# Kernel tuning notes

Hardware: AMD Instinct MI355X
Metric: run time of the kernel (lower is better)

Reference implementation:

```python
import jax, jax.numpy as jnp
import numpy as np

NUM_HEADS = 16
HEAD_DIM = 64
D_DEC = 1024
D_ENC = 1024
R = 256  # kv_lora_rank
LN_EPS = 1e-5


def setup_inputs() -> dict:
    key = jax.random.key(0)
    ks = jax.random.split(key, 8)
    B, SQ, SK = 4, 2048, 4096
    query = jax.random.normal(ks[0], (B, SQ, D_DEC), dtype=jnp.float32)
    encoder_output = jax.random.normal(ks[1], (B, SK, D_ENC), dtype=jnp.float32)
    s = 0.02
    Wq = jax.random.normal(ks[2], (NUM_HEADS * HEAD_DIM, D_DEC), dtype=jnp.float32) * s
    Wkva = jax.random.normal(ks[3], (R, D_ENC), dtype=jnp.float32) * s
    ln_g = jnp.ones((R,), dtype=jnp.float32)
    ln_b = jnp.zeros((R,), dtype=jnp.float32)
    Wkvb = jax.random.normal(ks[4], (NUM_HEADS * 2 * HEAD_DIM, R), dtype=jnp.float32) * s
    Wout = jax.random.normal(ks[5], (D_DEC, NUM_HEADS * HEAD_DIM), dtype=jnp.float32) * s
    return {"query": query, "encoder_output": encoder_output, "Wq": Wq,
            "Wkva": Wkva, "ln_g": ln_g, "ln_b": ln_b, "Wkvb": Wkvb, "Wout": Wout}


def reference(query, encoder_output, Wq, Wkva, ln_g, ln_b, Wkvb, Wout):
    B, SQ, _ = query.shape
    SK = encoder_output.shape[1]
    H, Dh = NUM_HEADS, HEAD_DIM

    # q projection -> [B, H, SQ, Dh]
    q = jnp.einsum('bsd,ed->bse', query, Wq).reshape(B, SQ, H, Dh).transpose(0, 2, 1, 3)

    # low-rank KV compression + layernorm
    c = jnp.einsum('bsd,rd->bsr', encoder_output, Wkva)  # [B, SK, R]
    mu = jnp.mean(c, axis=-1, keepdims=True)
    var = jnp.mean(jnp.square(c - mu), axis=-1, keepdims=True)
    c = (c - mu) * jax.lax.rsqrt(var + LN_EPS) * ln_g + ln_b

    # decompress to K,V: [B, SK, H, 2*Dh] -> split
    kv = jnp.einsum('bsr,er->bse', c, Wkvb).reshape(B, SK, H, 2 * Dh).transpose(0, 2, 1, 3)
    k, v = kv[..., :Dh], kv[..., Dh:]

    scale = 1.0 / np.sqrt(Dh).astype(np.float32)
    scores = jnp.einsum('bhqd,bhkd->bhqk', q, k) * scale
    attn = jax.nn.softmax(scores, axis=-1)  # dropout is identity in eval / p=0
    o = jnp.einsum('bhqk,bhkd->bhqd', attn, v)
    o = o.transpose(0, 2, 1, 3).reshape(B, SQ, H * Dh)
    return jnp.einsum('bse,de->bsd', o, Wout)
```

## Files before the change

### kernel.cpp

```cpp
#include <hip/hip_runtime.h>

#define LOG2E 1.4426950408889634f

typedef __attribute__((ext_vector_type(8))) short short8;
typedef __attribute__((ext_vector_type(4))) float f32x4;

__device__ inline unsigned short f2bf(float f) {
  unsigned u = __float_as_uint(f);
  u += 0x7fffu + ((u >> 16) & 1u);
  return (unsigned short)(u >> 16);
}

#define MFMA16(a, b, c) __builtin_amdgcn_mfma_f32_16x16x32_bf16((a), (b), (c), 0, 0, 0)

#define GLDS16(gp, lp)                                                              \
  __builtin_amdgcn_global_load_lds((const __attribute__((address_space(1))) void*)(gp), \
                                   (__attribute__((address_space(3))) void*)(lp), 16, 0, 0)

__device__ inline f32x4 zero4() {
  f32x4 z = {0.f, 0.f, 0.f, 0.f};
  return z;
}

__device__ inline int swz8(int row) { return (row ^ (row >> 3)) & 7; }

__global__ __launch_bounds__(256) void k_cast(const float* __restrict__ in,
                                              unsigned short* __restrict__ out, int n) {
  int i = (blockIdx.x * 256 + threadIdx.x) * 4;
  if (i >= n) return;
  float4 v = *(const float4*)(in + i);
  unsigned lo = (unsigned)f2bf(v.x) | ((unsigned)f2bf(v.y) << 16);
  unsigned hi = (unsigned)f2bf(v.z) | ((unsigned)f2bf(v.w) << 16);
  *(uint2*)(out + i) = make_uint2(lo, hi);
}

__global__ __launch_bounds__(256, 2) void k_qproj(const unsigned short* __restrict__ A,
                                                  const unsigned short* __restrict__ Bw,
                                                  unsigned short* __restrict__ Qout) {
  __shared__ __align__(16) short As[128 * 32];
  __shared__ __align__(16) short Bs[128 * 32];
  const int K = 1024;
  int tid = threadIdx.x;
  int w = tid >> 6, lane = tid & 63, quad = lane >> 4, c = lane & 15;
  int m0 = blockIdx.x * 128, n0 = blockIdx.y * 128;
  int wm = (w >> 1) * 64, wn = (w & 1) * 64;
  f32x4 acc[4][4];
#pragma unroll
  for (int i = 0; i < 4; i++)
#pragma unroll
    for (int j = 0; j < 4; j++) acc[i][j] = zero4();

  for (int k0 = 0; k0 < K; k0 += 32) {
#pragma unroll
    for (int i = 0; i < 2; i++) {
      int seg = w * 2 + i;
      int bo = seg * 1024 + lane * 16;
      int row = bo >> 6, col = (bo & 63) >> 1;
      GLDS16(A + (size_t)(m0 + row) * K + k0 + col, (char*)As + seg * 1024);
      GLDS16(Bw + (size_t)(n0 + row) * K + k0 + col, (char*)Bs + seg * 1024);
    }
    __syncthreads();
    short8 af[4], bfr[4];
#pragma unroll
    for (int i = 0; i < 4; i++) {
      af[i] = *(const short8*)&As[(wm + i * 16 + c) * 32 + quad * 8];
      bfr[i] = *(const short8*)&Bs[(wn + i * 16 + c) * 32 + quad * 8];
    }
#pragma unroll
    for (int mi = 0; mi < 4; mi++)
#pragma unroll
      for (int ni = 0; ni < 4; ni++) acc[mi][ni] = MFMA16(af[mi], bfr[ni], acc[mi][ni]);
    __syncthreads();
  }
  const float scale = 0.125f * LOG2E;
#pragma unroll
  for (int mi = 0; mi < 4; mi++) {
    int rowb = m0 + wm + mi * 16 + quad * 4;
#pragma unroll
    for (int ni = 0; ni < 4; ni++) {
      int col = n0 + wn + ni * 16 + c;
      int h = col >> 6, d = col & 63;
#pragma unroll
      for (int r = 0; r < 4; r++) {
        int row = rowb + r;
        int b = row >> 11, sq = row & 2047;
        Qout[(((size_t)(b * 16 + h)) * 2048 + sq) * 64 + d] = f2bf(acc[mi][ni][r] * scale);
      }
    }
  }
}

__global__ __launch_bounds__(256, 2) void k_cln(const unsigned short* __restrict__ E,
                                                const unsigned short* __restrict__ Wa,
                                                const float* __restrict__ g, const float* __restrict__ bb,
                                                unsigned short* __restrict__ Cout) {
  __shared__ __align__(16) short As[64 * 32];
  __shared__ __align__(16) short Bs[256 * 32];
  __shared__ float redS[4][64], redQ[4][64];
  __shared__ float gS[256], bS[256];
  const int K = 1024;
  int tid = threadIdx.x;
  int w = tid >> 6, lane = tid & 63, quad = lane >> 4, c = lane & 15;
  int m0 = blockIdx.x * 64;
  gS[tid] = g[tid];
  bS[tid] = bb[tid];
  f32x4 acc[4][4];
#pragma unroll
  for (int i = 0; i < 4; i++)
#pragma unroll
    for (int j = 0; j < 4; j++) acc[i][j] = zero4();

  for (int k0 = 0; k0 < K; k0 += 32) {
    {
      int bo = w * 1024 + lane * 16;
      int row = bo >> 6, col = (bo & 63) >> 1;
      GLDS16(E + (size_t)(m0 + row) * K + k0 + col, (char*)As + w * 1024);
    }
#pragma unroll
    for (int i = 0; i < 4; i++) {
      int seg = w * 4 + i;
      int bo = seg * 1024 + lane * 16;
      int row = bo >> 6, col = (bo & 63) >> 1;
      GLDS16(Wa + (size_t)row * K + k0 + col, (char*)Bs + seg * 1024);
    }
    __syncthreads();
    short8 af[4], bfr[4];
#pragma unroll
    for (int i = 0; i < 4; i++) {
      af[i] = *(const short8*)&As[(i * 16 + c) * 32 + quad * 8];
      bfr[i] = *(const short8*)&Bs[(w * 64 + i * 16 + c) * 32 + quad * 8];
    }
#pragma unroll
    for (int mi = 0; mi < 4; mi++)
#pragma unroll
      for (int ni = 0; ni < 4; ni++) acc[mi][ni] = MFMA16(af[mi], bfr[ni], acc[mi][ni]);
    __syncthreads();
  }
  float ps[4][4], pq[4][4];
#pragma unroll
  for (int mi = 0; mi < 4; mi++)
#pragma unroll
    for (int r = 0; r < 4; r++) {
      float s = 0.f, q = 0.f;
#pragma unroll
      for (int ni = 0; ni < 4; ni++) {
        float x = acc[mi][ni][r];
        s += x;
        q += x * x;
      }
      for (int m = 1; m < 16; m <<= 1) {
        s += __shfl_xor(s, m, 64);
        q += __shfl_xor(q, m, 64);
      }
      ps[mi][r] = s;
      pq[mi][r] = q;
    }
  if (c == 0) {
#pragma unroll
    for (int mi = 0; mi < 4; mi++)
#pragma unroll
      for (int r = 0; r < 4; r++) {
        int row = mi * 16 + quad * 4 + r;
        redS[w][row] = ps[mi][r];
        redQ[w][row] = pq[mi][r];
      }
  }
  __syncthreads();
  float muv[4][4], rsv[4][4];
#pragma unroll
  for (int mi = 0; mi < 4; mi++)
#pragma unroll
    for (int r = 0; r < 4; r++) {
      int row = mi * 16 + quad * 4 + r;
      float S = redS[0][row] + redS[1][row] + redS[2][row] + redS[3][row];
      float Q = redQ[0][row] + redQ[1][row] + redQ[2][row] + redQ[3][row];
      float mu = S * (1.f / 256.f);
      float var = Q * (1.f / 256.f) - mu * mu;
      muv[mi][r] = mu;
      rsv[mi][r] = rsqrtf(var + 1e-5f);
    }
#pragma unroll
  for (int mi = 0; mi < 4; mi++)
#pragma unroll
    for (int ni = 0; ni < 4; ni++) {
      int col = w * 64 + ni * 16 + c;
#pragma unroll
      for (int r = 0; r < 4; r++) {
        int row = m0 + mi * 16 + quad * 4 + r;
        float y = (acc[mi][ni][r] - muv[mi][r]) * rsv[mi][r] * gS[col] + bS[col];
        Cout[(size_t)row * 256 + col] = f2bf(y);
      }
    }
}

__global__ __launch_bounds__(256, 2) void k_kv(const unsigned short* __restrict__ A,
                                               const unsigned short* __restrict__ Bw,
                                               unsigned short* __restrict__ Kb,
                                               unsigned short* __restrict__ Vb) {
  __shared__ __align__(16) short As[128 * 32];
  __shared__ __align__(16) short Bs[128 * 32];
  const int K = 256;
  int tid = threadIdx.x;
  int w = tid >> 6, lane = tid & 63, quad = lane >> 4, c = lane & 15;
  int m0 = blockIdx.x * 128, n0 = blockIdx.y * 128;
  int wm = (w >> 1) * 64, wn = (w & 1) * 64;
  f32x4 acc[4][4];
#pragma unroll
  for (int i = 0; i < 4; i++)
#pragma unroll
    for (int j = 0; j < 4; j++) acc[i][j] = zero4();

  for (int k0 = 0; k0 < K; k0 += 32) {
#pragma unroll
    for (int i = 0; i < 2; i++) {
      int seg = w * 2 + i;
      int bo = seg * 1024 + lane * 16;
      int row = bo >> 6, col = (bo & 63) >> 1;
      GLDS16(A + (size_t)(m0 + row) * K + k0 + col, (char*)As + seg * 1024);
      GLDS16(Bw + (size_t)(n0 + row) * K + k0 + col, (char*)Bs + seg * 1024);
    }
    __syncthreads();
    short8 af[4], bfr[4];
#pragma unroll
    for (int i = 0; i < 4; i++) {
      af[i] = *(const short8*)&As[(wm + i * 16 + c) * 32 + quad * 8];
      bfr[i] = *(const short8*)&Bs[(wn + i * 16 + c) * 32 + quad * 8];
    }
#pragma unroll
    for (int mi = 0; mi < 4; mi++)
#pragma unroll
      for (int ni = 0; ni < 4; ni++) acc[mi][ni] = MFMA16(af[mi], bfr[ni], acc[mi][ni]);
    __syncthreads();
  }
#pragma unroll
  for (int mi = 0; mi < 4; mi++) {
    int rowb = m0 + wm + mi * 16 + quad * 4;
#pragma unroll
    for (int ni = 0; ni < 4; ni++) {
      int col = n0 + wn + ni * 16 + c;
      int h = col >> 7, rr = col & 127;
#pragma unroll
      for (int r = 0; r < 4; r++) {
        int row = rowb + r;
        int b = row >> 12, sk = row & 4095;
        float x = acc[mi][ni][r];
        if (rr < 64)
          Kb[(((size_t)(b * 16 + h)) * 4096 + sk) * 64 + rr] = f2bf(x);
        else
          Vb[(((size_t)(b * 16 + h)) * 64 + (rr - 64)) * 4096 + sk] = f2bf(x);
      }
    }
  }
}

__global__ __launch_bounds__(256, 2) void k_attn(const unsigned short* __restrict__ Qb,
                                                 const unsigned short* __restrict__ Kb,
                                                 const unsigned short* __restrict__ Vb,
                                                 unsigned short* __restrict__ Ob) {
  __shared__ __align__(16) short Qs[256 * 64];
  __shared__ __align__(16) short Ks[64 * 64];
  __shared__ __align__(16) short Vs[64 * 64];
  int tid = threadIdx.x;
  int w = tid >> 6, lane = tid & 63, quad = lane >> 4, c = lane & 15;
  int r8 = lane >> 3, pc = lane & 7;
  int bh = blockIdx.y, qt = blockIdx.x;
  const unsigned short* Qp = Qb + ((size_t)bh * 2048 + qt * 256) * 64;
  const unsigned short* Kp = Kb + (size_t)bh * 4096 * 64;
  const unsigned short* Vp = Vb + (size_t)bh * 64 * 4096;

#pragma unroll
  for (int i = 0; i < 8; i++) {
    int seg = w * 8 + i;
    int row = seg * 8 + r8;
    int lc = pc ^ swz8(row);
    GLDS16(Qp + (size_t)row * 64 + lc * 8, (char*)Qs + seg * 1024);
  }
  __syncthreads();
  short8 qf[4][2];
#pragma unroll
  for (int nt = 0; nt < 4; nt++) {
    int row = w * 64 + nt * 16 + c;
#pragma unroll
    for (int kk = 0; kk < 2; kk++)
      qf[nt][kk] = *(const short8*)((const char*)Qs + row * 128 + (((kk * 4 + quad) ^ swz8(row)) << 4));
  }
  char* PsW = (char*)Qs + w * 8192;

  f32x4 O[4][4];
  float lp[4] = {0.f, 0.f, 0.f, 0.f};
#pragma unroll
  for (int i = 0; i < 4; i++)
#pragma unroll
    for (int j = 0; j < 4; j++) O[i][j] = zero4();

  for (int kt = 0; kt < 64; kt++) {
#pragma unroll
    for (int i = 0; i < 4; i++) {
      int seg = w * 4 + i;
      if (seg < 8) {
        int row = seg * 8 + r8;
        int lc = pc ^ swz8(row);
        GLDS16(Kp + ((size_t)kt * 64 + row) * 64 + lc * 8, (char*)Ks + seg * 1024);
      } else {
        int row = (seg - 8) * 8 + r8;
        int lc = pc ^ swz8(row);
        GLDS16(Vp + (size_t)row * 4096 + kt * 64 + lc * 8, (char*)Vs + (seg - 8) * 1024);
      }
    }
    __syncthreads();

#pragma unroll
    for (int mt = 0; mt < 4; mt++) {
      int krow = mt * 16 + c;
      short8 kf0 = *(const short8*)((const char*)Ks + krow * 128 + ((quad ^ swz8(krow)) << 4));
      short8 kf1 = *(const short8*)((const char*)Ks + krow * 128 + (((4 + quad) ^ swz8(krow)) << 4));
      f32x4 s[4];
#pragma unroll
      for (int nt = 0; nt < 4; nt++) {
        s[nt] = MFMA16(kf0, qf[nt][0], zero4());
        s[nt] = MFMA16(kf1, qf[nt][1], s[nt]);
      }
#pragma unroll
      for (int nt = 0; nt < 4; nt++) {
        float p0 = __builtin_amdgcn_exp2f(s[nt][0]);
        float p1 = __builtin_amdgcn_exp2f(s[nt][1]);
        float p2 = __builtin_amdgcn_exp2f(s[nt][2]);
        float p3 = __builtin_amdgcn_exp2f(s[nt][3]);
        lp[nt] += (p0 + p1) + (p2 + p3);
        unsigned u0 = ((__float_as_uint(p0) + 0x8000u) >> 16) | ((__float_as_uint(p1) + 0x8000u) & 0xffff0000u);
        unsigned u1 = ((__float_as_uint(p2) + 0x8000u) >> 16) | ((__float_as_uint(p3) + 0x8000u) & 0xffff0000u);
        int prow = nt * 16 + c;
        int chunk = (mt * 2 + (quad >> 1)) ^ swz8(prow);
        *(uint2*)(PsW + prow * 128 + (chunk << 4) + (quad & 1) * 8) = make_uint2(u0, u1);
      }
    }

#pragma unroll
    for (int kk = 0; kk < 2; kk++) {
      short8 vf[4];
#pragma unroll
      for (int dt = 0; dt < 4; dt++) {
        int vrow = dt * 16 + c;
        vf[dt] = *(const short8*)((const char*)Vs + vrow * 128 + (((kk * 4 + quad) ^ swz8(vrow)) << 4));
      }
#pragma unroll
      for (int mo = 0; mo < 4; mo++) {
        int prow = mo * 16 + c;
        short8 pf = *(const short8*)((const char*)PsW + prow * 128 + (((kk * 4 + quad) ^ swz8(prow)) << 4));
#pragma unroll
        for (int dt = 0; dt < 4; dt++) O[mo][dt] = MFMA16(pf, vf[dt], O[mo][dt]);
      }
    }
    __syncthreads();
  }

#pragma unroll
  for (int nt = 0; nt < 4; nt++) {
    lp[nt] += __shfl_xor(lp[nt], 16, 64);
    lp[nt] += __shfl_xor(lp[nt], 32, 64);
  }
  int b = bh >> 4, h = bh & 15;
#pragma unroll
  for (int mo = 0; mo < 4; mo++) {
#pragma unroll
    for (int r = 0; r < 4; r++) {
      float inv = __builtin_amdgcn_rcpf(__shfl(lp[mo], quad * 4 + r, 64));
      int sq = qt * 256 + w * 64 + mo * 16 + quad * 4 + r;
#pragma unroll
      for (int dt = 0; dt < 4; dt++)
        Ob[((size_t)b * 2048 + sq) * 1024 + h * 64 + dt * 16 + c] = f2bf(O[mo][dt][r] * inv);
    }
  }
}

__global__ __launch_bounds__(256, 2) void k_out(const unsigned short* __restrict__ A,
                                                const unsigned short* __restrict__ Bw,
                                                float* __restrict__ Out) {
  __shared__ __align__(16) short As[128 * 32];
  __shared__ __align__(16) short Bs[128 * 32];
  const int K = 1024;
  int tid = threadIdx.x;
  int w = tid >> 6, lane = tid & 63, quad = lane >> 4, c = lane & 15;
  int m0 = blockIdx.x * 128, n0 = blockIdx.y * 128;
  int wm = (w >> 1) * 64, wn = (w & 1) * 64;
  f32x4 acc[4][4];
#pragma unroll
  for (int i = 0; i < 4; i++)
#pragma unroll
    for (int j = 0; j < 4; j++) acc[i][j] = zero4();

  for (int k0 = 0; k0 < K; k0 += 32) {
#pragma unroll
    for (int i = 0; i < 2; i++) {
      int seg = w * 2 + i;
      int bo = seg * 1024 + lane * 16;
      int row = bo >> 6, col = (bo & 63) >> 1;
      GLDS16(A + (size_t)(m0 + row) * K + k0 + col, (char*)As + seg * 1024);
      GLDS16(Bw + (size_t)(n0 + row) * K + k0 + col, (char*)Bs + seg * 1024);
    }
    __syncthreads();
    short8 af[4], bfr[4];
#pragma unroll
    for (int i = 0; i < 4; i++) {
      af[i] = *(const short8*)&As[(wm + i * 16 + c) * 32 + quad * 8];
      bfr[i] = *(const short8*)&Bs[(wn + i * 16 + c) * 32 + quad * 8];
    }
#pragma unroll
    for (int mi = 0; mi < 4; mi++)
#pragma unroll
      for (int ni = 0; ni < 4; ni++) acc[mi][ni] = MFMA16(af[mi], bfr[ni], acc[mi][ni]);
    __syncthreads();
  }
#pragma unroll
  for (int mi = 0; mi < 4; mi++) {
    int rowb = m0 + wm + mi * 16 + quad * 4;
#pragma unroll
    for (int ni = 0; ni < 4; ni++) {
      int col = n0 + wn + ni * 16 + c;
#pragma unroll
      for (int r = 0; r < 4; r++) Out[(size_t)(rowb + r) * 1024 + col] = acc[mi][ni][r];
    }
  }
}

extern "C" void kernel_launch(void* const* d_in, const int* in_sizes, int n_in,
                              void* d_out, int out_size, void* d_ws, size_t ws_size,
                              hipStream_t stream) {
  const float* query = (const float*)d_in[0];
  const float* enc = (const float*)d_in[1];
  const float* Wq = (const float*)d_in[2];
  const float* Wkva = (const float*)d_in[3];
  const float* ln_g = (const float*)d_in[4];
  const float* ln_b = (const float*)d_in[5];
  const float* Wkvb = (const float*)d_in[6];
  const float* Wout = (const float*)d_in[7];
  if (ws_size < 81264640) return;

  char* ws = (char*)d_ws;
  unsigned short* wq_bf = (unsigned short*)(ws + 0);
  unsigned short* wa_bf = (unsigned short*)(ws + 2097152);
  unsigned short* wb_bf = (unsigned short*)(ws + 2621440);
  unsigned short* wo_bf = (unsigned short*)(ws + 3670016);
  unsigned short* qproj = (unsigned short*)(ws + 5767168);
  unsigned short* cln = (unsigned short*)(ws + 22544384);
  unsigned short* ebf_v = (unsigned short*)(ws + 30932992);
  unsigned short* qin_o = (unsigned short*)(ws + 64487424);
  unsigned short* kbuf = (unsigned short*)d_out;

  k_cast<<<1024, 256, 0, stream>>>(Wq, wq_bf, 1048576);
  k_cast<<<256, 256, 0, stream>>>(Wkva, wa_bf, 262144);
  k_cast<<<512, 256, 0, stream>>>(Wkvb, wb_bf, 524288);
  k_cast<<<1024, 256, 0, stream>>>(Wout, wo_bf, 1048576);
  k_cast<<<8192, 256, 0, stream>>>(query, qin_o, 8388608);
  k_cast<<<16384, 256, 0, stream>>>(enc, ebf_v, 16777216);

  k_qproj<<<dim3(64, 8), 256, 0, stream>>>(qin_o, wq_bf, qproj);
  k_cln<<<256, 256, 0, stream>>>(ebf_v, wa_bf, ln_g, ln_b, cln);
  k_kv<<<dim3(128, 16), 256, 0, stream>>>(cln, wb_bf, kbuf, ebf_v);
  k_attn<<<dim3(8, 64), 256, 0, stream>>>(qproj, kbuf, ebf_v, qin_o);
  k_out<<<dim3(64, 8), 256, 0, stream>>>(qin_o, wo_bf, (float*)d_out);
}
```

Baseline: 470.3 us.

## Double-buffer K/V tiles in attention and merge bf16 cast launches

The attention kernel now holds two K/V LDS buffers. It prefetches the next key tile with async global-to-LDS loads while computing on the current one, which drops the barrier that sat between each load and its use. Separately, the six float-to-bf16 cast launches are merged into one kernel that picks its source by flat index, cutting launch overhead. The cost is more LDS per block (64KB instead of 48KB), which could limit occupancy, plus a little branching in the cast kernel.

```diff
diff --git a/kernel.cpp b/kernel.cpp
--- a/kernel.cpp
+++ b/kernel.cpp
@@ -24,14 +24,25 @@
 
 __device__ inline int swz8(int row) { return (row ^ (row >> 3)) & 7; }
 
-__global__ __launch_bounds__(256) void k_cast(const float* __restrict__ in,
-                                              unsigned short* __restrict__ out, int n) {
+__global__ __launch_bounds__(256) void k_cast6(
+    const float* __restrict__ e, const float* __restrict__ q, const float* __restrict__ wq,
+    const float* __restrict__ wo, const float* __restrict__ wb, const float* __restrict__ wa,
+    unsigned short* __restrict__ eo, unsigned short* __restrict__ qo, unsigned short* __restrict__ wqo,
+    unsigned short* __restrict__ woo, unsigned short* __restrict__ wbo, unsigned short* __restrict__ wao) {
   int i = (blockIdx.x * 256 + threadIdx.x) * 4;
-  if (i >= n) return;
-  float4 v = *(const float4*)(in + i);
+  const float* src;
+  unsigned short* dst;
+  int off;
+  if (i < 16777216) { src = e; dst = eo; off = i; }
+  else if (i < 25165824) { src = q; dst = qo; off = i - 16777216; }
+  else if (i < 26214400) { src = wq; dst = wqo; off = i - 25165824; }
+  else if (i < 27262976) { src = wo; dst = woo; off = i - 26214400; }
+  else if (i < 27787264) { src = wb; dst = wbo; off = i - 27262976; }
+  else { src = wa; dst = wao; off = i - 27787264; }
+  float4 v = *(const float4*)(src + off);
   unsigned lo = (unsigned)f2bf(v.x) | ((unsigned)f2bf(v.y) << 16);
   unsigned hi = (unsigned)f2bf(v.z) | ((unsigned)f2bf(v.w) << 16);
-  *(uint2*)(out + i) = make_uint2(lo, hi);
+  *(uint2*)(dst + off) = make_uint2(lo, hi);
 }
 
 __global__ __launch_bounds__(256, 2) void k_qproj(const unsigned short* __restrict__ A,
@@ -258,8 +269,7 @@
                                                  const unsigned short* __restrict__ Vb,
                                                  unsigned short* __restrict__ Ob) {
   __shared__ __align__(16) short Qs[256 * 64];
-  __shared__ __align__(16) short Ks[64 * 64];
-  __shared__ __align__(16) short Vs[64 * 64];
+  __shared__ __align__(16) short KVs[2][2 * 64 * 64];
   int tid = threadIdx.x;
   int w = tid >> 6, lane = tid & 63, quad = lane >> 4, c = lane & 15;
   int r8 = lane >> 3, pc = lane & 7;
@@ -275,6 +285,16 @@
     int lc = pc ^ swz8(row);
     GLDS16(Qp + (size_t)row * 64 + lc * 8, (char*)Qs + seg * 1024);
   }
+#pragma unroll
+  for (int i = 0; i < 4; i++) {
+    int seg = w * 4 + i;
+    int row = (seg & 7) * 8 + r8;
+    int lc = pc ^ swz8(row);
+    if (seg < 8)
+      GLDS16(Kp + (size_t)row * 64 + lc * 8, (char*)KVs[0] + seg * 1024);
+    else
+      GLDS16(Vp + (size_t)row * 4096 + lc * 8, (char*)KVs[0] + seg * 1024);
+  }
   __syncthreads();
   short8 qf[4][2];
 #pragma unroll
@@ -294,26 +314,27 @@
     for (int j = 0; j < 4; j++) O[i][j] = zero4();
 
   for (int kt = 0; kt < 64; kt++) {
-#pragma unroll
-    for (int i = 0; i < 4; i++) {
-      int seg = w * 4 + i;
-      if (seg < 8) {
-        int row = seg * 8 + r8;
+    const char* KsC = (const char*)KVs[kt & 1];
+    const char* VsC = KsC + 8192;
+    if (kt < 63) {
+      char* nb = (char*)KVs[(kt + 1) & 1];
+#pragma unroll
+      for (int i = 0; i < 4; i++) {
+        int seg = w * 4 + i;
+        int row = (seg & 7) * 8 + r8;
         int lc = pc ^ swz8(row);
-        GLDS16(Kp + ((size_t)kt * 64 + row) * 64 + lc * 8, (char*)Ks + seg * 1024);
-      } else {
-        int row = (seg - 8) * 8 + r8;
-        int lc = pc ^ swz8(row);
-        GLDS16(Vp + (size_t)row * 4096 + kt * 64 + lc * 8, (char*)Vs + (seg - 8) * 1024);
-      }
-    }
-    __syncthreads();
+        if (seg < 8)
+          GLDS16(Kp + ((size_t)(kt + 1) * 64 + row) * 64 + lc * 8, nb + seg * 1024);
+        else
+          GLDS16(Vp + (size_t)row * 4096 + (kt + 1) * 64 + lc * 8, nb + seg * 1024);
+      }
+    }
 
 #pragma unroll
     for (int mt = 0; mt < 4; mt++) {
       int krow = mt * 16 + c;
-      short8 kf0 = *(const short8*)((const char*)Ks + krow * 128 + ((quad ^ swz8(krow)) << 4));
-      short8 kf1 = *(const short8*)((const char*)Ks + krow * 128 + (((4 + quad) ^ swz8(krow)) << 4));
+      short8 kf0 = *(const short8*)(KsC + krow * 128 + ((quad ^ swz8(krow)) << 4));
+      short8 kf1 = *(const short8*)(KsC + krow * 128 + (((4 + quad) ^ swz8(krow)) << 4));
       f32x4 s[4];
 #pragma unroll
       for (int nt = 0; nt < 4; nt++) {
@@ -341,7 +362,7 @@
 #pragma unroll
       for (int dt = 0; dt < 4; dt++) {
         int vrow = dt * 16 + c;
-        vf[dt] = *(const short8*)((const char*)Vs + vrow * 128 + (((kk * 4 + quad) ^ swz8(vrow)) << 4));
+        vf[dt] = *(const short8*)(VsC + vrow * 128 + (((kk * 4 + quad) ^ swz8(vrow)) << 4));
       }
 #pragma unroll
       for (int mo = 0; mo < 4; mo++) {
@@ -447,12 +468,8 @@
   unsigned short* qin_o = (unsigned short*)(ws + 64487424);
   unsigned short* kbuf = (unsigned short*)d_out;
 
-  k_cast<<<1024, 256, 0, stream>>>(Wq, wq_bf, 1048576);
-  k_cast<<<256, 256, 0, stream>>>(Wkva, wa_bf, 262144);
-  k_cast<<<512, 256, 0, stream>>>(Wkvb, wb_bf, 524288);
-  k_cast<<<1024, 256, 0, stream>>>(Wout, wo_bf, 1048576);
-  k_cast<<<8192, 256, 0, stream>>>(query, qin_o, 8388608);
-  k_cast<<<16384, 256, 0, stream>>>(enc, ebf_v, 16777216);
+  k_cast6<<<27392, 256, 0, stream>>>(enc, query, Wq, Wout, Wkvb, Wkva,
+                                     ebf_v, qin_o, wq_bf, wo_bf, wb_bf, wa_bf);
 
   k_qproj<<<dim3(64, 8), 256, 0, stream>>>(qin_o, wq_bf, qproj);
   k_cln<<<256, 256, 0, stream>>>(ebf_v, wa_bf, ln_g, ln_b, cln);
```

Result: faster. 460.7 us (-2.0%).
